# Optimization experiments

Hardware: AMD Instinct MI355X
Metric: run time of the kernel (lower is better)

## Reference

```python
import math
import jax, jax.numpy as jnp
import numpy as np

B, NV, C = 8, 512, 256
H, R = 6, 32
PAIR_H = 16
RBF_K = 8


def setup_inputs() -> dict:
    key = jax.random.key(0)
    ks = jax.random.split(key, 12)
    s = lambda fan_in: 1.0 / math.sqrt(fan_in)
    inp = {
        'feats': jax.random.normal(ks[0], (B, 2 * NV + 1, C), jnp.float32),
        'xy': jax.random.uniform(ks[1], (B, NV, 2), jnp.float32),
        'Wq': jax.random.normal(ks[2], (C, H * R), jnp.float32) * s(C),
        'Wk': jax.random.normal(ks[3], (C, H * R), jnp.float32) * s(C),
        'Wpi': jax.random.normal(ks[4], (C, PAIR_H), jnp.float32) * s(C),
        'bpi': jnp.zeros((PAIR_H,), jnp.float32),
        'Wpj': jax.random.normal(ks[5], (C, PAIR_H), jnp.float32) * s(C),
        'bpj': jnp.zeros((PAIR_H,), jnp.float32),
        'gW1': jax.random.normal(ks[6], (2 + RBF_K + 2, 32), jnp.float32) * s(12),
        'gb1': jnp.zeros((32,), jnp.float32),
        'gW2': jax.random.normal(ks[7], (32, 1), jnp.float32) * s(32),
        'gb2': jnp.zeros((1,), jnp.float32),
        'aW1': jax.random.normal(ks[8], (6, 16), jnp.float32) * s(6),
        'ab1': jnp.zeros((16,), jnp.float32),
        'aW2': jax.random.normal(ks[9], (16, 1), jnp.float32) * s(16),
        'ab2': jnp.zeros((1,), jnp.float32),
        'dW': jax.random.normal(ks[10], (C, 1), jnp.float32) * s(C),
        'db': jnp.zeros((1,), jnp.float32),
        'alpha_pair': jnp.float32(0.5),
        'alpha_geom': jnp.float32(0.6),
        'alpha_angle': jnp.float32(0.6),
        'logit_scale': jnp.float32(1.0),
    }
    return inp


def _pos_scale(p, lo=0.0, hi=1.5):
    return lo + (hi - lo) * jax.nn.sigmoid(p)


def _logit_scale_fn(p, lo=0.5, hi=3.0):
    return lo + (hi - lo) * jax.nn.sigmoid(p)


def reference(feats, xy, Wq, Wk, Wpi, bpi, Wpj, bpj, gW1, gb1, gW2, gb2,
              aW1, ab1, aW2, ab2, dW, db,
              alpha_pair, alpha_geom, alpha_angle, logit_scale):
    # fold vertices: drop BOS, average (y, x) token pairs -> [B, N, C]
    x = feats[:, 1:]
    Bb, L, Cc = x.shape
    x = x.reshape(Bb, L // 2, 2, Cc).mean(axis=2)
    N = x.shape[1]

    # multi-head low-rank bilinear core, summed over heads
    Q = (x @ Wq).reshape(Bb, N, H, R)
    K = (x @ Wk).reshape(Bb, N, H, R)
    S = jnp.einsum('bnhr,bmhr->bnm', Q, K) / math.sqrt(R)

    # separable pair nonlinearity (outer product of tiny ReLU features)
    a_i = jax.nn.relu(x @ Wpi + bpi)
    b_j = jax.nn.relu(x @ Wpj + bpj)
    S = S + _pos_scale(alpha_pair) * jnp.einsum('bnd,bmd->bnm', a_i, b_j)

    # geometry / angle biases
    yv, xv = xy[..., 0], xy[..., 1]
    dy = yv[:, :, None] - yv[:, None, :]          # [B,N,N]
    dx = xv[:, :, None] - xv[:, None, :]
    theta = jnp.arctan2(dy, dx)
    pad_i = (jnp.abs(yv) < 1e-9) & (jnp.abs(xv) < 1e-9)
    pad_pair = pad_i[:, :, None] | pad_i[:, None, :]
    c1, s1 = jnp.cos(theta), jnp.sin(theta)

    # distance RBF + cos/sin bias
    rbf_mu = jnp.linspace(0.0, math.sqrt(2.0), RBF_K).astype(jnp.float32)
    spacing = rbf_mu[1] - rbf_mu[0]
    rbf_gamma = 1.0 / (2.0 * spacing ** 2 + 1e-8)
    r = jnp.sqrt(dy * dy + dx * dx + 1e-8)
    phi = jnp.exp(-rbf_gamma * (r[..., None] - rbf_mu) ** 2)  # [B,N,N,K]
    geom_feat = jnp.concatenate(
        [dy[..., None], dx[..., None], phi, c1[..., None], s1[..., None]], axis=-1)
    G = (jax.nn.relu(geom_feat @ gW1 + gb1) @ gW2 + gb2)[..., 0]
    G = jnp.where(pad_pair, 0.0, G)
    S = S + _pos_scale(alpha_geom) * G

    # angle harmonics (theta, 2theta, 4theta)
    c2, s2 = jnp.cos(2.0 * theta), jnp.sin(2.0 * theta)
    c4, s4 = jnp.cos(4.0 * theta), jnp.sin(4.0 * theta)
    ang_feat = jnp.stack([c1, s1, c2, s2, c4, s4], axis=-1)  # [B,N,N,6]
    Hb = (jax.nn.relu(ang_feat @ aW1 + ab1) @ aW2 + ab2)[..., 0]
    Hb = jnp.where(pad_pair, 0.0, Hb)
    S = S + _pos_scale(alpha_angle) * Hb

    # diagonal bias and bounded global scale
    d = (x @ dW + db)[..., 0]                     # [B,N]
    idx = jnp.arange(N)
    S = S.at[:, idx, idx].add(d)
    S = S * _logit_scale_fn(logit_scale)
    return S
```

## Files before the change

kernel.cpp:

```cpp
#include <hip/hip_runtime.h>
#include <math.h>


#define UK 224

typedef __attribute__((ext_vector_type(8)))  short short8;
typedef __attribute__((ext_vector_type(16))) float f32x16;
typedef __attribute__((ext_vector_type(4)))  int   int4v;

__device__ __forceinline__ float sigmoidf_(float x){ return 1.0f/(1.0f + __expf(-x)); }
__device__ __forceinline__ unsigned f2bf(float x){
    unsigned u = __builtin_bit_cast(unsigned, x);
    return (u + 0x7fffu + ((u>>16)&1u)) >> 16;
}
__device__ __forceinline__ unsigned pk2(float lo, float hi){
    unsigned r;
    asm("v_cvt_pk_bf16_f32 %0, %1, %2" : "=v"(r) : "v"(lo), "v"(hi));
    return r;
}
__device__ __forceinline__ f32x16 zero16(){
    f32x16 z;
    #pragma unroll
    for (int i = 0; i < 16; i++) z[i] = 0.f;
    return z;
}

__global__ __launch_bounds__(256) void k_prep(const float* __restrict__ feats,
        const float* __restrict__ Wq, const float* __restrict__ Wk,
        const float* __restrict__ Wpi, const float* __restrict__ bpi,
        const float* __restrict__ Wpj, const float* __restrict__ bpj,
        const float* __restrict__ dW, const float* __restrict__ db,
        const float* __restrict__ a_pair,
        unsigned short* __restrict__ xb, unsigned short* __restrict__ WT,
        float* __restrict__ bcat){
    int blk = blockIdx.x, tid = threadIdx.x;
    if (blk < 4096){
        int b = blk >> 9, n = blk & 511;
        size_t base = ((size_t)(b*1025 + 1 + 2*n))*256 + tid;
        float v = 0.5f*(feats[base] + feats[base+256]);
        xb[(size_t)blk*256 + tid] = (unsigned short)f2bf(v);
    } else {
        int col = blk - 4096;
        int c   = tid;
        const float invSqrtR = 0.17677669529663687f;
        float sp = 1.5f*sigmoidf_(a_pair[0]);
        float v;
        if      (col < 192)  v = Wq[c*192 + col]*invSqrtR;
        else if (col < 208)  v = sp*Wpi[c*16 + (col-192)];
        else if (col < 400)  v = Wk[c*192 + (col-208)];
        else if (col < 416)  v = Wpj[c*16 + (col-400)];
        else if (col == 416) v = dW[c];
        else v = 0.f;
        WT[col*256 + c] = (unsigned short)f2bf(v);
        if (tid == 0){
            float bv = 0.f;
            if      (col >= 192 && col < 208) bv = sp*bpi[col-192];
            else if (col >= 400 && col < 416) bv = bpj[col-400];
            else if (col == 416)              bv = db[0];
            bcat[col] = bv;
        }
    }
}

__global__ __launch_bounds__(256) void k_uv(const unsigned short* __restrict__ xb,
        const unsigned short* __restrict__ WT, const float* __restrict__ bcat,
        unsigned short* __restrict__ Ub, unsigned short* __restrict__ Vb,
        float* __restrict__ dv){
    int tid = threadIdx.x;
    int lane = tid & 63, l31 = lane & 31, hf = lane >> 5;
    int w = tid >> 6, wr = w >> 1, wc = w & 1;
    int c0 = blockIdx.x*64, r0 = blockIdx.y*64;
    const unsigned short* ap = xb + (size_t)(r0 + wr*32 + l31)*256 + 8*hf;
    const unsigned short* bp = WT + (size_t)(c0 + wc*32 + l31)*256 + 8*hf;
    f32x16 acc = zero16();
    #pragma unroll 4
    for (int k0 = 0; k0 < 256; k0 += 16){
        short8 a  = *(const short8*)(ap + k0);
        short8 bb = *(const short8*)(bp + k0);
        acc = __builtin_amdgcn_mfma_f32_32x32x16_bf16(a, bb, acc, 0, 0, 0);
    }
    int col = c0 + wc*32 + l31;
    int rb  = r0 + wr*32 + 4*hf;
    float bc = bcat[col];
    #pragma unroll
    for (int r = 0; r < 16; r++){
        int row = rb + (r&3) + 8*(r>>2);
        float v = acc[r] + bc;
        size_t ui = (size_t)row*UK;
        if (col < 208){
            if (col >= 192) v = fmaxf(v, 0.f);
            Ub[ui + col] = (unsigned short)f2bf(v);
        } else if (col < 224){
            Vb[ui + col-208] = (unsigned short)f2bf(v);
            Ub[ui + col] = 0;
        } else if (col < 416){
            if (col >= 400) v = fmaxf(v, 0.f);
            Vb[ui + col-208] = (unsigned short)f2bf(v);
        } else if (col == 416){
            dv[row] = v;
            Vb[ui + 208] = 0;
        } else if (col < 432){
            Vb[ui + col-208] = 0;
        }
    }
}

__global__ __launch_bounds__(256) void k_gemm(const unsigned short* __restrict__ Ub,
        const unsigned short* __restrict__ Vb, float* __restrict__ S){
    int tid = threadIdx.x;
    int lane = tid & 63, l31 = lane & 31, hf = lane >> 5;
    int w = tid >> 6, wr = w >> 1, wc = w & 1;
    int b = blockIdx.z;
    int m0 = blockIdx.x*64, n0 = blockIdx.y*64;
    const unsigned short* ap = Ub + (size_t)(b*512 + n0 + wr*32 + l31)*UK + 8*hf;
    const unsigned short* bp = Vb + (size_t)(b*512 + m0 + wc*32 + l31)*UK + 8*hf;
    f32x16 acc = zero16();
    #pragma unroll 2
    for (int k0 = 0; k0 < UK; k0 += 16){
        short8 a  = *(const short8*)(ap + k0);
        short8 bb = *(const short8*)(bp + k0);
        acc = __builtin_amdgcn_mfma_f32_32x32x16_bf16(a, bb, acc, 0, 0, 0);
    }
    int m  = m0 + wc*32 + l31;
    int nb = n0 + wr*32 + 4*hf;
    float* Sp = S + ((size_t)b*512)*512 + m;
    #pragma unroll
    for (int r = 0; r < 16; r++){
        int n = nb + (r&3) + 8*(r>>2);
        Sp[(size_t)n*512] = acc[r];
    }
}

__global__ __launch_bounds__(256, 3) void k_pairs(const float* __restrict__ xy,
        const float* __restrict__ gW1, const float* __restrict__ gb1,
        const float* __restrict__ gW2, const float* __restrict__ gb2,
        const float* __restrict__ aW1, const float* __restrict__ ab1,
        const float* __restrict__ aW2, const float* __restrict__ ab2,
        const float* __restrict__ dv,
        const float* __restrict__ a_geom, const float* __restrict__ a_ang,
        const float* __restrict__ lsc,
        float* __restrict__ S){
    int tid  = threadIdx.x;
    int lane = tid & 63;
    int hf   = lane >> 5;
    int l31  = lane & 31;

    float sg = 1.5f*sigmoidf_(a_geom[0]);
    float sa = 1.5f*sigmoidf_(a_ang[0]);
    float ls = 0.5f + 2.5f*sigmoidf_(lsc[0]);

    short8 wg, wa;
    #pragma unroll
    for (int j = 0; j < 8; j++){
        int f = hf*8 + j;
        float vg = (f < 12) ? gW1[f*32 + l31] : 0.f;
        float va = (f >= 10 && l31 < 16) ? aW1[(f-10)*16 + l31] : 0.f;
        wg[j] = (short)f2bf(vg);
        wa[j] = (short)f2bf(va);
    }

    float nbg[16], g2g[16], nba[16], g2a[16];
    float bsum = 0.f;
    #pragma unroll
    for (int r = 0; r < 16; r++){
        int h = (r&3) + 8*(r>>2) + 4*hf;
        float bg  = gb1[h];
        float wg2 = sg*gW2[h];
        nbg[r] = -bg; g2g[r] = wg2; bsum += bg*wg2;
        if (h < 16){
            float ba  = ab1[h];
            float wa2 = sa*aW2[h];
            nba[r] = -ba; g2a[r] = wa2; bsum += ba*wa2;
        } else { nba[r] = 0.f; g2a[r] = 0.f; }
    }
    bsum += __shfl_xor(bsum, 32);
    float cb = sg*gb2[0] + sa*ab2[0] + bsum;

    const float GAMMA = 12.2499985f;
    const float TWOGD = 4.9497469f;

    int wid = __builtin_amdgcn_readfirstlane(tid >> 6);
    int wave_g = blockIdx.x*4 + wid;
    for (int c = wave_g; c < 32768; c += 8192){
        int base = c*64;
        int nn = (base >> 9) & 511;
        int bb = base >> 18;
        const float* xyb = xy + (size_t)bb*1024;
        float yn = xyb[2*nn], xn = xyb[2*nn+1];
        bool padn = (fabsf(yn) < 1e-9f) && (fabsf(xn) < 1e-9f);
        float sv  = S[(size_t)base + lane];
        float dvn = dv[bb*512 + nn];
        int m_w = (base + lane) & 511;
        float ddg = (m_w == nn) ? dvn : 0.f;

        float2 pm = *(const float2*)(xyb + 2*m_w);
        float ym = pm.x, xm = pm.y;
        bool padm = (fabsf(ym) < 1e-9f) && (fabsf(xm) < 1e-9f);
        float msk = (padn || padm) ? 0.f : 1.f;
        float dy = yn - ym, dx = xn - xm;
        float r2 = dy*dy + dx*dx;
        float re = sqrtf(r2 + 1e-8f);
        float c1, s1;
        if (r2 > 0.f){ float inv = rsqrtf(r2); c1 = dx*inv; s1 = dy*inv; }
        else { c1 = 1.f; s1 = 0.f; }
        float c2 = c1*c1 - s1*s1, s2 = 2.f*c1*s1;
        float c4 = c2*c2 - s2*s2, s4 = 2.f*c2*s2;
        float e0 = __expf(-GAMMA*(r2 + 1e-8f));
        float E  = __expf(TWOGD*re);
        float u  = e0;
        float p0 = u;
        u *= E; float p1 = 0.60653066f*u;
        u *= E; float p2 = 0.13533528f*u;
        u *= E; float p3 = 0.011108997f*u;
        u *= E; float p4 = 3.3546263e-4f*u;
        u *= E; float p5 = 3.7266532e-6f*u;
        u *= E; float p6 = 1.5229979e-8f*u;
        u *= E; float p7 = 2.2897348e-11f*u;
        unsigned pk0 = pk2(dy, dx), pk1 = pk2(p0, p1), pk2_ = pk2(p2, p3), pk3 = pk2(p4, p5);
        unsigned pk4 = pk2(p6, p7), pk5 = pk2(c1, s1), pk6 = pk2(c2, s2), pk7 = pk2(c4, s4);

        int s0 = __shfl_xor((int)(hf ? pk0 : pk4), 32);
        int s1i= __shfl_xor((int)(hf ? pk1 : pk5), 32);
        int s2i= __shfl_xor((int)(hf ? pk2_: pk6), 32);
        int s3i= __shfl_xor((int)(hf ? pk3 : pk7), 32);

        int fA0 = hf ? s0 : (int)pk0, fA1 = hf ? s1i : (int)pk1;
        int fA2 = hf ? s2i : (int)pk2_, fA3 = hf ? s3i : (int)pk3;
        int fB0 = hf ? (int)pk4 : s0,  fB1 = hf ? (int)pk5 : s1i;
        int fB2 = hf ? (int)pk6 : s2i, fB3 = hf ? (int)pk7 : s3i;
        int4v ivA = {fA0, fA1, fA2, fA3};
        int4v ivB = {fB0, fB1, fB2, fB3};
        short8 bfA = __builtin_bit_cast(short8, ivA);
        short8 bfB = __builtin_bit_cast(short8, ivB);

        f32x16 z = zero16();
        f32x16 dgA = __builtin_amdgcn_mfma_f32_32x32x16_bf16(wg, bfA, z, 0, 0, 0);
        f32x16 dgB = __builtin_amdgcn_mfma_f32_32x32x16_bf16(wg, bfB, z, 0, 0, 0);
        f32x16 daA = __builtin_amdgcn_mfma_f32_32x32x16_bf16(wa, bfA, z, 0, 0, 0);
        f32x16 daB = __builtin_amdgcn_mfma_f32_32x32x16_bf16(wa, bfB, z, 0, 0, 0);

        float a0=0.f,a1=0.f,a2=0.f,a3=0.f,b0=0.f,b1=0.f,b2=0.f,b3=0.f;
        #pragma unroll
        for (int r = 0; r < 8; r++){
            a0 += fmaxf(dgA[r],   nbg[r])   * g2g[r];
            a1 += fmaxf(dgA[r+8], nbg[r+8]) * g2g[r+8];
            b0 += fmaxf(dgB[r],   nbg[r])   * g2g[r];
            b1 += fmaxf(dgB[r+8], nbg[r+8]) * g2g[r+8];
            a2 += fmaxf(daA[r],   nba[r])   * g2a[r];
            a3 += fmaxf(daA[r+8], nba[r+8]) * g2a[r+8];
            b2 += fmaxf(daB[r],   nba[r])   * g2a[r];
            b3 += fmaxf(daB[r+8], nba[r+8]) * g2a[r+8];
        }
        float accA = (a0 + a1) + (a2 + a3);
        float accB = (b0 + b1) + (b2 + b3);
        accA += __shfl_xor(accA, 32);
        accB += __shfl_xor(accB, 32);

        float res = (lane < 32) ? accA : accB;
        S[(size_t)base + lane] = (sv + msk*(res + cb) + ddg) * ls;
    }
}

extern "C" void kernel_launch(void* const* d_in, const int* in_sizes, int n_in,
                              void* d_out, int out_size, void* d_ws, size_t ws_size,
                              hipStream_t stream){
    const float* feats = (const float*)d_in[0];
    const float* xy    = (const float*)d_in[1];
    const float* Wq    = (const float*)d_in[2];
    const float* Wk    = (const float*)d_in[3];
    const float* Wpi   = (const float*)d_in[4];
    const float* bpi   = (const float*)d_in[5];
    const float* Wpj   = (const float*)d_in[6];
    const float* bpj   = (const float*)d_in[7];
    const float* gW1   = (const float*)d_in[8];
    const float* gb1   = (const float*)d_in[9];
    const float* gW2   = (const float*)d_in[10];
    const float* gb2   = (const float*)d_in[11];
    const float* aW1   = (const float*)d_in[12];
    const float* ab1   = (const float*)d_in[13];
    const float* aW2   = (const float*)d_in[14];
    const float* ab2   = (const float*)d_in[15];
    const float* dW    = (const float*)d_in[16];
    const float* db    = (const float*)d_in[17];
    const float* a_pair= (const float*)d_in[18];
    const float* a_geom= (const float*)d_in[19];
    const float* a_ang = (const float*)d_in[20];
    const float* lsc   = (const float*)d_in[21];

    float* S = (float*)d_out;
    char* wsb = (char*)d_ws;
    unsigned short* xb = (unsigned short*)wsb;
    unsigned short* WT = (unsigned short*)(wsb + 2097152);
    unsigned short* Ub = (unsigned short*)(wsb + 2326528);
    unsigned short* Vb = (unsigned short*)(wsb + 4161536);
    float* bcat = (float*)(wsb + 5996544);
    float* dv   = (float*)(wsb + 5998336);

    k_prep <<<4544, 256, 0, stream>>>(feats, Wq, Wk, Wpi, bpi, Wpj, bpj, dW, db, a_pair,
                                      xb, WT, bcat);
    k_uv   <<<dim3(7,64), 256, 0, stream>>>(xb, WT, bcat, Ub, Vb, dv);
    k_gemm <<<dim3(8,8,8), 256, 0, stream>>>(Ub, Vb, S);
    k_pairs<<<2048, 256, 0, stream>>>(xy, gW1, gb1, gW2, gb2, aW1, ab1, aW2, ab2,
                                      dv, a_geom, a_ang, lsc, S);
}
```

Before: 53.80 us.

## Fuse bilinear GEMM and pairwise geometry/angle bias into one tiled kernel

Merges the MFMA GEMM kernel and the pairwise MLP bias kernel into a single kernel over 64x64 output tiles. The GEMM result is held in shared memory, the geometry and angle bias is added in place, and the final scaled tile, including the diagonal term, is written once. This removes a full write and re-read of the 8x512x512 float S matrix and one kernel launch. In exchange the grid drops to 512 blocks of 4 waves with a 16 KB LDS tile each, which may leave the MLP-heavy pairwise phase with less parallelism than the old 2048-block launch.

```diff
diff --git a/kernel.cpp b/kernel.cpp
--- a/kernel.cpp
+++ b/kernel.cpp
@@ -105,33 +105,8 @@
     }
 }
 
-__global__ __launch_bounds__(256) void k_gemm(const unsigned short* __restrict__ Ub,
-        const unsigned short* __restrict__ Vb, float* __restrict__ S){
-    int tid = threadIdx.x;
-    int lane = tid & 63, l31 = lane & 31, hf = lane >> 5;
-    int w = tid >> 6, wr = w >> 1, wc = w & 1;
-    int b = blockIdx.z;
-    int m0 = blockIdx.x*64, n0 = blockIdx.y*64;
-    const unsigned short* ap = Ub + (size_t)(b*512 + n0 + wr*32 + l31)*UK + 8*hf;
-    const unsigned short* bp = Vb + (size_t)(b*512 + m0 + wc*32 + l31)*UK + 8*hf;
-    f32x16 acc = zero16();
-    #pragma unroll 2
-    for (int k0 = 0; k0 < UK; k0 += 16){
-        short8 a  = *(const short8*)(ap + k0);
-        short8 bb = *(const short8*)(bp + k0);
-        acc = __builtin_amdgcn_mfma_f32_32x32x16_bf16(a, bb, acc, 0, 0, 0);
-    }
-    int m  = m0 + wc*32 + l31;
-    int nb = n0 + wr*32 + 4*hf;
-    float* Sp = S + ((size_t)b*512)*512 + m;
-    #pragma unroll
-    for (int r = 0; r < 16; r++){
-        int n = nb + (r&3) + 8*(r>>2);
-        Sp[(size_t)n*512] = acc[r];
-    }
-}
-
-__global__ __launch_bounds__(256, 3) void k_pairs(const float* __restrict__ xy,
+__global__ __launch_bounds__(256, 3) void k_gp(const unsigned short* __restrict__ Ub,
+        const unsigned short* __restrict__ Vb, const float* __restrict__ xy,
         const float* __restrict__ gW1, const float* __restrict__ gb1,
         const float* __restrict__ gW2, const float* __restrict__ gb2,
         const float* __restrict__ aW1, const float* __restrict__ ab1,
@@ -140,10 +115,30 @@
         const float* __restrict__ a_geom, const float* __restrict__ a_ang,
         const float* __restrict__ lsc,
         float* __restrict__ S){
-    int tid  = threadIdx.x;
-    int lane = tid & 63;
-    int hf   = lane >> 5;
-    int l31  = lane & 31;
+    __shared__ float acc_lds[64][64];
+    int tid = threadIdx.x;
+    int lane = tid & 63, l31 = lane & 31, hf = lane >> 5;
+    int w = tid >> 6, wr = w >> 1, wc = w & 1;
+    int b = blockIdx.z;
+    int m0 = blockIdx.x*64, n0 = blockIdx.y*64;
+
+    {
+        const unsigned short* ap = Ub + (size_t)(b*512 + n0 + wr*32 + l31)*UK + 8*hf;
+        const unsigned short* bp = Vb + (size_t)(b*512 + m0 + wc*32 + l31)*UK + 8*hf;
+        f32x16 acc = zero16();
+        #pragma unroll 2
+        for (int k0 = 0; k0 < UK; k0 += 16){
+            short8 a  = *(const short8*)(ap + k0);
+            short8 bb = *(const short8*)(bp + k0);
+            acc = __builtin_amdgcn_mfma_f32_32x32x16_bf16(a, bb, acc, 0, 0, 0);
+        }
+        int colL = wc*32 + l31;
+        int rbL  = wr*32 + 4*hf;
+        #pragma unroll
+        for (int r = 0; r < 16; r++)
+            acc_lds[rbL + (r&3) + 8*(r>>2)][colL] = acc[r];
+    }
+    __syncthreads();
 
     float sg = 1.5f*sigmoidf_(a_geom[0]);
     float sa = 1.5f*sigmoidf_(a_ang[0]);
@@ -158,7 +153,6 @@
         wg[j] = (short)f2bf(vg);
         wa[j] = (short)f2bf(va);
     }
-
     float nbg[16], g2g[16], nba[16], g2a[16];
     float bsum = 0.f;
     #pragma unroll
@@ -178,25 +172,20 @@
 
     const float GAMMA = 12.2499985f;
     const float TWOGD = 4.9497469f;
-
-    int wid = __builtin_amdgcn_readfirstlane(tid >> 6);
-    int wave_g = blockIdx.x*4 + wid;
-    for (int c = wave_g; c < 32768; c += 8192){
-        int base = c*64;
-        int nn = (base >> 9) & 511;
-        int bb = base >> 18;
-        const float* xyb = xy + (size_t)bb*1024;
+    const float* xyb = xy + (size_t)b*1024;
+
+    int m_w = m0 + lane;
+    float2 pmv = *(const float2*)(xyb + 2*m_w);
+    float ym = pmv.x, xm = pmv.y;
+    bool padm = (fabsf(ym) < 1e-9f) && (fabsf(xm) < 1e-9f);
+
+    for (int i = 0; i < 16; i++){
+        int nrow = (w << 4) + i;
+        int nn = n0 + nrow;
         float yn = xyb[2*nn], xn = xyb[2*nn+1];
         bool padn = (fabsf(yn) < 1e-9f) && (fabsf(xn) < 1e-9f);
-        float sv  = S[(size_t)base + lane];
-        float dvn = dv[bb*512 + nn];
-        int m_w = (base + lane) & 511;
-        float ddg = (m_w == nn) ? dvn : 0.f;
-
-        float2 pm = *(const float2*)(xyb + 2*m_w);
-        float ym = pm.x, xm = pm.y;
-        bool padm = (fabsf(ym) < 1e-9f) && (fabsf(xm) < 1e-9f);
         float msk = (padn || padm) ? 0.f : 1.f;
+
         float dy = yn - ym, dx = xn - xm;
         float r2 = dy*dy + dx*dx;
         float re = sqrtf(r2 + 1e-8f);
@@ -257,7 +246,22 @@
         accB += __shfl_xor(accB, 32);
 
         float res = (lane < 32) ? accA : accB;
-        S[(size_t)base + lane] = (sv + msk*(res + cb) + ddg) * ls;
+        acc_lds[nrow][lane] += msk*(res + cb);
+    }
+    __syncthreads();
+
+    {
+        int m  = m0 + wc*32 + l31;
+        int rbL = wr*32 + 4*hf;
+        float* Sp = S + ((size_t)b*512)*512 + m;
+        #pragma unroll
+        for (int r = 0; r < 16; r++){
+            int nloc = rbL + (r&3) + 8*(r>>2);
+            int n = n0 + nloc;
+            float v = acc_lds[nloc][wc*32 + l31];
+            if (m == n) v += dv[b*512 + n];
+            Sp[(size_t)n*512] = v * ls;
+        }
     }
 }
 
@@ -299,7 +303,7 @@
     k_prep <<<4544, 256, 0, stream>>>(feats, Wq, Wk, Wpi, bpi, Wpj, bpj, dW, db, a_pair,
                                       xb, WT, bcat);
     k_uv   <<<dim3(7,64), 256, 0, stream>>>(xb, WT, bcat, Ub, Vb, dv);
-    k_gemm <<<dim3(8,8,8), 256, 0, stream>>>(Ub, Vb, S);
-    k_pairs<<<2048, 256, 0, stream>>>(xy, gW1, gb1, gW2, gb2, aW1, ab1, aW2, ab2,
-                                      dv, a_geom, a_ang, lsc, S);
-}
+    k_gp   <<<dim3(8,8,8), 256, 0, stream>>>(Ub, Vb, xy, gW1, gb1, gW2, gb2,
+                                             aW1, ab1, aW2, ab2, dv,
+                                             a_geom, a_ang, lsc, S);
+}
```

Measured after the change: 52.07 us. -3.2%, faster.
